# Optimization experiments

Measured on AMD Instinct MI355X. Metric: run time of the kernel, lower is better.

## Reference

```python
import jax, jax.numpy as jnp
import numpy as np

INPUT_DEM = 2048
HS_DEM = 2048


def setup_inputs() -> dict:
    key = jax.random.key(0)
    ks = jax.random.split(key, 10)
    d, h = INPUT_DEM, HS_DEM
    inp = {
        "x": jax.random.normal(ks[0], (d,), dtype=jnp.float32),
        "w_xi": jax.random.normal(ks[1], (d, h), dtype=jnp.float32) * 0.01,
        "w_xf": jax.random.normal(ks[2], (d, h), dtype=jnp.float32) * 0.01,
        "w_xo": jax.random.normal(ks[3], (d, h), dtype=jnp.float32) * 0.01,
        "w_xc": jax.random.normal(ks[4], (d, h), dtype=jnp.float32) * 0.01,
        "w_hi": jax.random.normal(ks[5], (h, h), dtype=jnp.float32) * 0.01,
        "w_hf": jax.random.normal(ks[6], (h, h), dtype=jnp.float32) * 0.01,
        "w_ho": jax.random.normal(ks[7], (h, h), dtype=jnp.float32) * 0.01,
        "w_hc": jax.random.normal(ks[8], (h, h), dtype=jnp.float32) * 0.01,
        "b_i": jnp.zeros((h,), dtype=jnp.float32),
        "b_f": jnp.zeros((h,), dtype=jnp.float32),
        "b_o": jnp.zeros((h,), dtype=jnp.float32),
        "b_c": jnp.zeros((h,), dtype=jnp.float32),
        "h0": jnp.zeros((h,), dtype=jnp.float32),  # initial hidden_state
        "c0": jnp.zeros((h,), dtype=jnp.float32),  # initial cell_state
    }
    return inp


def reference(x, w_xi, w_xf, w_xo, w_xc, w_hi, w_hf, w_ho, w_hc,
              b_i, b_f, b_o, b_c, h0, c0):
    # gate = sigmoid(x @ Wx + h @ Wh + b)  (four GEMVs per gate pair)
    def gate(wx, wh, b):
        return jax.nn.sigmoid(x @ wx + h0 @ wh + b)

    i = gate(w_xi, w_hi, b_i)
    f = gate(w_xf, w_hf, b_f)
    o = gate(w_xo, w_ho, b_o)
    c = gate(w_xc, w_hc, b_c)

    # NOTE: original uses torch.dot(i, c) -> SCALAR, broadcast over cell state
    cell = f * c0 + jnp.dot(i, c)
    # inline normalization; torch.std is unbiased (ddof=1)
    cell = (cell - cell.mean()) / (jnp.std(cell, ddof=1) + 1e-5)
    h = o * jnp.tanh(cell)
    return h
```

## Files before the change

### kernel.cpp

```cpp
#include <hip/hip_runtime.h>
#include <math.h>

#define HS    2048
#define DIN   2048
#define RPS   32
#define NSLAB (DIN / RPS)
#define NBLK1 256
#define NBLK2 64

typedef float float4n __attribute__((ext_vector_type(4)));

__global__ __launch_bounds__(256) void gemv_slab(
        const float* __restrict__ x,    const float* __restrict__ h0,
        const float* __restrict__ w_xf, const float* __restrict__ w_hf,
        const float* __restrict__ w_xo, const float* __restrict__ w_ho,
        float* __restrict__ zp ) {
    const int b    = blockIdx.x;
    const int t    = threadIdx.x;
    const int mat  = b >> 6;
    const int slab = b & (NSLAB - 1);

    const float* W   = (mat == 0) ? w_xf : (mat == 1) ? w_hf
                     : (mat == 2) ? w_xo : w_ho;
    const float* vec = (mat & 1) ? h0 : x;

    const int r0 = slab * RPS;
    const float4n* wp = reinterpret_cast<const float4n*>(W + (size_t)r0 * HS) + t;

    float4n a0 = {0.f, 0.f, 0.f, 0.f};
    float4n a1 = {0.f, 0.f, 0.f, 0.f};
    float4n a2 = {0.f, 0.f, 0.f, 0.f};
    float4n a3 = {0.f, 0.f, 0.f, 0.f};
#pragma unroll
    for (int r = 0; r < RPS; r += 2) {
        const float s0 = vec[r0 + r];
        const float s1 = vec[r0 + r + 1];
        const float4n w00 = __builtin_nontemporal_load(wp + (size_t)r * (HS / 4));
        const float4n w01 = __builtin_nontemporal_load(wp + (size_t)r * (HS / 4) + 256);
        const float4n w10 = __builtin_nontemporal_load(wp + (size_t)(r + 1) * (HS / 4));
        const float4n w11 = __builtin_nontemporal_load(wp + (size_t)(r + 1) * (HS / 4) + 256);
        a0 += s0 * w00;
        a1 += s0 * w01;
        a2 += s1 * w10;
        a3 += s1 * w11;
    }
    const float4n q0 = a0 + a2;
    const float4n q1 = a1 + a3;
    float4n* zrow = reinterpret_cast<float4n*>(zp + (size_t)b * HS);
    zrow[t]       = q0;
    zrow[256 + t] = q1;
}

__global__ __launch_bounds__(256) void reduce_fin(
        const float* __restrict__ zp,
        const float* __restrict__ b_f, const float* __restrict__ b_o,
        const float* __restrict__ c0,  float* __restrict__ out,
        float* __restrict__ vbuf, float* __restrict__ obuf,
        unsigned* __restrict__ cnt) {
    const int t  = threadIdx.x;
    const int g  = blockIdx.x >> 5;
    const int cg = blockIdx.x & 31;
    const int fg = t & 15;
    const int ph = t >> 4;

    __shared__ float4 part[4][16];
    __shared__ unsigned lastFlag;

    const int colq = cg * 64 + fg * 4;

    float4 acc0 = make_float4(0.f, 0.f, 0.f, 0.f);
    float4 acc1 = make_float4(0.f, 0.f, 0.f, 0.f);
#pragma unroll
    for (int k = 0; k < 8; k += 2) {
        const int row0 = g * 128 + ph + (k << 4);
        const int row1 = g * 128 + ph + ((k + 1) << 4);
        const float4 p0 = *reinterpret_cast<const float4*>(
            zp + (size_t)row0 * HS + colq);
        const float4 p1 = *reinterpret_cast<const float4*>(
            zp + (size_t)row1 * HS + colq);
        acc0.x += p0.x;  acc0.y += p0.y;  acc0.z += p0.z;  acc0.w += p0.w;
        acc1.x += p1.x;  acc1.y += p1.y;  acc1.z += p1.z;  acc1.w += p1.w;
    }
    float4 s4;
    s4.x = acc0.x + acc1.x;  s4.y = acc0.y + acc1.y;
    s4.z = acc0.z + acc1.z;  s4.w = acc0.w + acc1.w;

#pragma unroll
    for (int m = 16; m <= 32; m <<= 1) {
        s4.x += __shfl_xor(s4.x, m);
        s4.y += __shfl_xor(s4.y, m);
        s4.z += __shfl_xor(s4.z, m);
        s4.w += __shfl_xor(s4.w, m);
    }
    if ((t & 63) < 16) part[t >> 6][fg] = s4;
    __syncthreads();

    if (t < 16) {
        float4 z;
        z.x = (part[0][t].x + part[1][t].x) + (part[2][t].x + part[3][t].x);
        z.y = (part[0][t].y + part[1][t].y) + (part[2][t].y + part[3][t].y);
        z.z = (part[0][t].z + part[1][t].z) + (part[2][t].z + part[3][t].z);
        z.w = (part[0][t].w + part[1][t].w) + (part[2][t].w + part[3][t].w);
        const int col = cg * 64 + t * 4;
        if (g == 0) {
            const float4 bf = *reinterpret_cast<const float4*>(b_f + col);
            const float4 cv = *reinterpret_cast<const float4*>(c0 + col);
            float4 r;
            r.x = cv.x / (1.f + expf(-(z.x + bf.x)));
            r.y = cv.y / (1.f + expf(-(z.y + bf.y)));
            r.z = cv.z / (1.f + expf(-(z.z + bf.z)));
            r.w = cv.w / (1.f + expf(-(z.w + bf.w)));
            *reinterpret_cast<float4*>(vbuf + col) = r;
        } else {
            const float4 bo = *reinterpret_cast<const float4*>(b_o + col);
            float4 r;
            r.x = 1.f / (1.f + expf(-(z.x + bo.x)));
            r.y = 1.f / (1.f + expf(-(z.y + bo.y)));
            r.z = 1.f / (1.f + expf(-(z.z + bo.z)));
            r.w = 1.f / (1.f + expf(-(z.w + bo.w)));
            *reinterpret_cast<float4*>(obuf + col) = r;
        }
    }
    __syncthreads();

    if (t == 0) {
        __threadfence();
        const unsigned old = atomicInc(cnt, NBLK2 - 1u);
        lastFlag = (old == NBLK2 - 2u);
    }
    __syncthreads();
    if (!lastFlag) return;
    __threadfence();

    const int lane = t & 63;
    const int wv   = t >> 6;
    __shared__ float red[2][4];

    float v[8], og[8];
    float lsum = 0.f;
#pragma unroll
    for (int e = 0; e < 8; ++e) {
        const int j = t * 8 + e;
        v[e]  = vbuf[j];
        og[e] = obuf[j];
        lsum += v[e];
    }
#pragma unroll
    for (int s = 32; s > 0; s >>= 1) lsum += __shfl_down(lsum, s);
    if (lane == 0) red[0][wv] = lsum;
    __syncthreads();
    const float mean = (red[0][0] + red[0][1] + red[0][2] + red[0][3]) * (1.f / 2048.f);

    float lss = 0.f;
#pragma unroll
    for (int e = 0; e < 8; ++e) {
        const float d = v[e] - mean;
        lss += d * d;
    }
#pragma unroll
    for (int s = 32; s > 0; s >>= 1) lss += __shfl_down(lss, s);
    if (lane == 0) red[1][wv] = lss;
    __syncthreads();
    const float var = (red[1][0] + red[1][1] + red[1][2] + red[1][3]) * (1.f / 2047.f);
    const float inv = 1.f / (sqrtf(var) + 1e-5f);

#pragma unroll
    for (int e = 0; e < 8; ++e) {
        const int j = t * 8 + e;
        out[j] = og[e] * tanhf((v[e] - mean) * inv);
    }
}

extern "C" void kernel_launch(void* const* d_in, const int* in_sizes, int n_in,
                              void* d_out, int out_size, void* d_ws, size_t ws_size,
                              hipStream_t stream) {
    const float* x    = (const float*)d_in[0];
    const float* w_xf = (const float*)d_in[2];
    const float* w_xo = (const float*)d_in[3];
    const float* w_hf = (const float*)d_in[6];
    const float* w_ho = (const float*)d_in[7];
    const float* b_f  = (const float*)d_in[10];
    const float* b_o  = (const float*)d_in[11];
    const float* h0   = (const float*)d_in[13];
    const float* c0   = (const float*)d_in[14];
    float* out = (float*)d_out;

    float* zp     = (float*)d_ws;
    float* vbuf   = zp + (size_t)NBLK1 * HS;
    float* obuf   = vbuf + HS;
    unsigned* cnt = (unsigned*)(obuf + HS);

    gemv_slab<<<NBLK1, 256, 0, stream>>>(x, h0, w_xf, w_hf, w_xo, w_ho, zp);
    reduce_fin<<<NBLK2, 256, 0, stream>>>(zp, b_f, b_o, c0, out, vbuf, obuf, cnt);
}
```

Measured before the change: 20.81 us.

## Fuse GEMV and reduction kernels into one launch with atomic grid barrier

Merges the slab GEMV kernel and the partial-sum reduction kernel into a single kernel. The last 64 blocks to arrive at an atomic counter spin until every block has finished, then run the reduction and finalization, which removes one kernel launch and the gap between launches. The spin-wait depends on all 256 blocks being resident at the same time, and those 64 blocks sit idle while the slowest blocks finish. A second counter picks the final normalizing block.

Measured after the change: 76.19 us. 266% more time.

```diff
diff --git a/kernel.cpp b/kernel.cpp
--- a/kernel.cpp
+++ b/kernel.cpp
@@ -5,61 +5,76 @@
 #define DIN   2048
 #define RPS   32
 #define NSLAB (DIN / RPS)
-#define NBLK1 256
-#define NBLK2 64
+#define NBLK  256
+#define NRED  64
 
 typedef float float4n __attribute__((ext_vector_type(4)));
 
-__global__ __launch_bounds__(256) void gemv_slab(
+__global__ __launch_bounds__(256) void lstm_fused(
         const float* __restrict__ x,    const float* __restrict__ h0,
         const float* __restrict__ w_xf, const float* __restrict__ w_hf,
         const float* __restrict__ w_xo, const float* __restrict__ w_ho,
-        float* __restrict__ zp ) {
-    const int b    = blockIdx.x;
-    const int t    = threadIdx.x;
-    const int mat  = b >> 6;
-    const int slab = b & (NSLAB - 1);
-
-    const float* W   = (mat == 0) ? w_xf : (mat == 1) ? w_hf
-                     : (mat == 2) ? w_xo : w_ho;
-    const float* vec = (mat & 1) ? h0 : x;
-
-    const int r0 = slab * RPS;
-    const float4n* wp = reinterpret_cast<const float4n*>(W + (size_t)r0 * HS) + t;
-
-    float4n a0 = {0.f, 0.f, 0.f, 0.f};
-    float4n a1 = {0.f, 0.f, 0.f, 0.f};
-    float4n a2 = {0.f, 0.f, 0.f, 0.f};
-    float4n a3 = {0.f, 0.f, 0.f, 0.f};
-#pragma unroll
-    for (int r = 0; r < RPS; r += 2) {
-        const float s0 = vec[r0 + r];
-        const float s1 = vec[r0 + r + 1];
-        const float4n w00 = __builtin_nontemporal_load(wp + (size_t)r * (HS / 4));
-        const float4n w01 = __builtin_nontemporal_load(wp + (size_t)r * (HS / 4) + 256);
-        const float4n w10 = __builtin_nontemporal_load(wp + (size_t)(r + 1) * (HS / 4));
-        const float4n w11 = __builtin_nontemporal_load(wp + (size_t)(r + 1) * (HS / 4) + 256);
-        a0 += s0 * w00;
-        a1 += s0 * w01;
-        a2 += s1 * w10;
-        a3 += s1 * w11;
-    }
-    const float4n q0 = a0 + a2;
-    const float4n q1 = a1 + a3;
-    float4n* zrow = reinterpret_cast<float4n*>(zp + (size_t)b * HS);
-    zrow[t]       = q0;
-    zrow[256 + t] = q1;
-}
-
-__global__ __launch_bounds__(256) void reduce_fin(
-        const float* __restrict__ zp,
-        const float* __restrict__ b_f, const float* __restrict__ b_o,
-        const float* __restrict__ c0,  float* __restrict__ out,
+        const float* __restrict__ b_f,  const float* __restrict__ b_o,
+        const float* __restrict__ c0,   float* __restrict__ out,
+        float* __restrict__ zp ,
         float* __restrict__ vbuf, float* __restrict__ obuf,
-        unsigned* __restrict__ cnt) {
-    const int t  = threadIdx.x;
-    const int g  = blockIdx.x >> 5;
-    const int cg = blockIdx.x & 31;
+        unsigned* __restrict__ cnt, unsigned* __restrict__ cnt2) {
+    const int b = blockIdx.x;
+    const int t = threadIdx.x;
+
+    {
+        const int mat  = b >> 6;
+        const int slab = b & (NSLAB - 1);
+        const float* W   = (mat == 0) ? w_xf : (mat == 1) ? w_hf
+                         : (mat == 2) ? w_xo : w_ho;
+        const float* vec = (mat & 1) ? h0 : x;
+
+        const int r0 = slab * RPS;
+        const float4n* wp =
+            reinterpret_cast<const float4n*>(W + (size_t)r0 * HS) + t;
+
+        float4n a0 = {0.f, 0.f, 0.f, 0.f};
+        float4n a1 = {0.f, 0.f, 0.f, 0.f};
+        float4n a2 = {0.f, 0.f, 0.f, 0.f};
+        float4n a3 = {0.f, 0.f, 0.f, 0.f};
+#pragma unroll
+        for (int r = 0; r < RPS; r += 2) {
+            const float s0 = vec[r0 + r];
+            const float s1 = vec[r0 + r + 1];
+            const float4n w00 = __builtin_nontemporal_load(wp + (size_t)r * (HS / 4));
+            const float4n w01 = __builtin_nontemporal_load(wp + (size_t)r * (HS / 4) + 256);
+            const float4n w10 = __builtin_nontemporal_load(wp + (size_t)(r + 1) * (HS / 4));
+            const float4n w11 = __builtin_nontemporal_load(wp + (size_t)(r + 1) * (HS / 4) + 256);
+            a0 += s0 * w00;
+            a1 += s0 * w01;
+            a2 += s1 * w10;
+            a3 += s1 * w11;
+        }
+        const float4n q0 = a0 + a2;
+        const float4n q1 = a1 + a3;
+        float4n* zrow = reinterpret_cast<float4n*>(zp + (size_t)b * HS);
+        zrow[t]       = q0;
+        zrow[256 + t] = q1;
+    }
+
+    __shared__ unsigned shOld;
+    __threadfence();
+    __syncthreads();
+    if (t == 0) shOld = atomicInc(cnt, NBLK - 1u);
+    __syncthreads();
+    const unsigned old = shOld;
+
+    if (old < NBLK - 65u || old > NBLK - 2u) return;
+    const int slice = (int)(old - (NBLK - 65u));
+
+    if (t == 0) {
+        while (atomicAdd(cnt, 0u) != NBLK - 1u) __builtin_amdgcn_s_sleep(1);
+    }
+    __syncthreads();
+    __threadfence();
+
+    const int g  = slice >> 5;
+    const int cg = slice & 31;
     const int fg = t & 15;
     const int ph = t >> 4;
 
@@ -121,12 +136,12 @@
             *reinterpret_cast<float4*>(obuf + col) = r;
         }
     }
-    __syncthreads();
-
+
+    __threadfence();
+    __syncthreads();
     if (t == 0) {
-        __threadfence();
-        const unsigned old = atomicInc(cnt, NBLK2 - 1u);
-        lastFlag = (old == NBLK2 - 2u);
+        const unsigned old2 = atomicInc(cnt2, NRED - 1u);
+        lastFlag = (old2 == NRED - 2u);
     }
     __syncthreads();
     if (!lastFlag) return;
@@ -185,11 +200,13 @@
     const float* c0   = (const float*)d_in[14];
     float* out = (float*)d_out;
 
-    float* zp     = (float*)d_ws;
-    float* vbuf   = zp + (size_t)NBLK1 * HS;
-    float* obuf   = vbuf + HS;
-    unsigned* cnt = (unsigned*)(obuf + HS);
-
-    gemv_slab<<<NBLK1, 256, 0, stream>>>(x, h0, w_xf, w_hf, w_xo, w_ho, zp);
-    reduce_fin<<<NBLK2, 256, 0, stream>>>(zp, b_f, b_o, c0, out, vbuf, obuf, cnt);
+    float* zp      = (float*)d_ws;
+    float* vbuf    = zp + (size_t)NBLK * HS;
+    float* obuf    = vbuf + HS;
+    unsigned* cnt  = (unsigned*)(obuf + HS);
+    unsigned* cnt2 = cnt + 1;
+
+    lstm_fused<<<NBLK, 256, 0, stream>>>(x, h0, w_xf, w_hf, w_xo, w_ho,
+                                         b_f, b_o, c0, out, zp, vbuf, obuf,
+                                         cnt, cnt2);
 }
```
